# Performance work log

Hardware: AMD Instinct MI355X
Metric: run time of the kernel (lower is better)

The kernel has to match this reference:

```python
import jax, jax.numpy as jnp
import numpy as np

D = 1024      # model_dim (input_dim)
H = 2048      # hidden_size_per_expert (hardcoded in module)
E = 8         # num_experts
K = 2         # topk
T = 8192      # tokens (batch after view)


def setup_inputs() -> dict:
    key = jax.random.key(0)
    ks = jax.random.split(key, 6)
    s_in = 1.0 / np.sqrt(D)
    s_h = 1.0 / np.sqrt(H)
    return {
        "x": jax.random.normal(ks[0], (T, D), dtype=jnp.float32),
        "wg": jax.random.normal(ks[1], (D, E), dtype=jnp.float32) * s_in,   # gate Linear(D,E,bias=False)
        "w1": jax.random.normal(ks[2], (E, D, H), dtype=jnp.float32) * s_in,
        "b1": jnp.zeros((E, H), dtype=jnp.float32),
        "w2": jax.random.normal(ks[3], (E, H, D), dtype=jnp.float32) * s_h,
        "b2": jnp.zeros((E, D), dtype=jnp.float32),
    }


def _moe(x, wg, w1, b1, w2, b2):
    # top-k gating (Tutel 'top' gate, k=K)
    logits = x @ wg                         # [T,E]
    scores = jax.nn.softmax(logits, -1)     # [T,E]
    topv, topi = jax.lax.top_k(scores, K)   # [T,K]
    sel = jax.nn.one_hot(topi, E, dtype=x.dtype)          # [T,K,E]
    combine = jnp.einsum('tk,tke->te', topv, sel)          # sparse combine weights [T,E]
    # GShard-style load-balance aux loss (top-1 dispatch mask)
    ce = sel[:, 0, :].mean(0)               # fraction of tokens whose top1 is e
    me = scores.mean(0)                     # mean gate prob per expert
    l_aux = jnp.sum(me * ce) * E
    # expert FFN (dense over experts; combine zeros out non-selected)
    h = jax.nn.relu(jnp.einsum('td,edh->teh', x, w1) + b1)  # [T,E,H]
    y = jnp.einsum('teh,ehd->ted', h, w2) + b2              # [T,E,D]
    out = jnp.einsum('te,ted->td', combine, y)              # [T,D]
    return out, l_aux


def reference(x, wg, w1, b1, w2, b2):
    return _moe(x, wg, w1, b1, w2, b2)
```

## Files before the change

kernel.cpp:

```cpp
#include <hip/hip_runtime.h>
#include <stdint.h>

#define T_TOK 8192
#define DIM   1024
#define HID   2048
#define NE    8

#define BM 128
#define BN 128
#define BK 64

#define GB_TOK 32

typedef float floatx4 __attribute__((ext_vector_type(4)));
typedef short shortx8 __attribute__((ext_vector_type(8)));

typedef __attribute__((address_space(3))) void       lds_void;
typedef const __attribute__((address_space(1))) void gbl_void;

__device__ __forceinline__ unsigned short f2bf(float f) {
  unsigned int u = __float_as_uint(f);
  unsigned int r = 0x7fffu + ((u >> 16) & 1u);
  return (unsigned short)((u + r) >> 16);
}

__global__ __launch_bounds__(256) void transpose_cast_kernel(const float* __restrict__ in,
                                                             unsigned short* __restrict__ out,
                                                             int R, int C) {
  __shared__ float tile[32][33];
  const size_t eoff = (size_t)blockIdx.z * R * C;
  const float* ip = in + eoff;
  unsigned short* op = out + eoff;
  int c0 = blockIdx.x * 32, r0 = blockIdx.y * 32;
  int tx = threadIdx.x, ty = threadIdx.y;
#pragma unroll
  for (int i = 0; i < 4; i++)
    tile[ty + i * 8][tx] = ip[(size_t)(r0 + ty + i * 8) * C + (c0 + tx)];
  __syncthreads();
#pragma unroll
  for (int i = 0; i < 4; i++)
    op[(size_t)(c0 + ty + i * 8) * R + (r0 + tx)] = f2bf(tile[tx][ty + i * 8]);
}

__global__ __launch_bounds__(256) void gate_kernel(const float* __restrict__ x,
                                                   const float* __restrict__ wg,
                                                   unsigned short* __restrict__ xb,
                                                   int* counts, int* top1cnt, float* ssum,
                                                   int* tok_list, float* wgt_list) {
  __shared__ int   lds_cnt[8];
  __shared__ int   lds_top1[8];
  __shared__ float lds_ssum[4][8];
  __shared__ int   tk_e[GB_TOK][2];
  __shared__ int   tk_r[GB_TOK][2];
  __shared__ float tk_w[GB_TOK][2];
  __shared__ int   base[8];

  const int tid = threadIdx.x;
  const int wave = tid >> 6;
  const int lane = tid & 63;

  if (tid < 8) { lds_cnt[tid] = 0; lds_top1[tid] = 0; }
  if (tid < 32) lds_ssum[tid >> 3][tid & 7] = 0.f;
  __syncthreads();

  float ssum_local[8];
#pragma unroll
  for (int e = 0; e < 8; e++) ssum_local[e] = 0.f;

  for (int it = 0; it < GB_TOK / 4; it++) {
    const int lt = it * 4 + wave;
    const int t = blockIdx.x * GB_TOK + lt;

    float acc[8];
#pragma unroll
    for (int e = 0; e < 8; e++) acc[e] = 0.f;
    const float* xr = x + (size_t)t * DIM;
    unsigned short* xw = xb + (size_t)t * DIM;
#pragma unroll
    for (int i = 0; i < 16; i++) {
      int d = i * 64 + lane;
      float xv = xr[d];
      xw[d] = f2bf(xv);
      const float4* wr = reinterpret_cast<const float4*>(wg + d * 8);
      float4 w0 = wr[0], w1 = wr[1];
      acc[0] += xv * w0.x; acc[1] += xv * w0.y; acc[2] += xv * w0.z; acc[3] += xv * w0.w;
      acc[4] += xv * w1.x; acc[5] += xv * w1.y; acc[6] += xv * w1.z; acc[7] += xv * w1.w;
    }
#pragma unroll
    for (int e = 0; e < 8; e++) {
#pragma unroll
      for (int off = 32; off > 0; off >>= 1) acc[e] += __shfl_xor(acc[e], off, 64);
    }
    if (lane == 0) {
      float mx = acc[0];
#pragma unroll
      for (int e = 1; e < 8; e++) mx = fmaxf(mx, acc[e]);
      float s[8], sum = 0.f;
#pragma unroll
      for (int e = 0; e < 8; e++) { s[e] = expf(acc[e] - mx); sum += s[e]; }
      float inv = 1.f / sum;
#pragma unroll
      for (int e = 0; e < 8; e++) { s[e] *= inv; ssum_local[e] += s[e]; }
      int i1 = 0;
#pragma unroll
      for (int e = 1; e < 8; e++) if (s[e] > s[i1]) i1 = e;
      int i2 = (i1 == 0) ? 1 : 0;
#pragma unroll
      for (int e = 0; e < 8; e++) if (e != i1 && s[e] > s[i2]) i2 = e;
      atomicAdd(&lds_top1[i1], 1);
      int r1 = atomicAdd(&lds_cnt[i1], 1);
      int r2 = atomicAdd(&lds_cnt[i2], 1);
      tk_e[lt][0] = i1; tk_r[lt][0] = r1; tk_w[lt][0] = s[i1];
      tk_e[lt][1] = i2; tk_r[lt][1] = r2; tk_w[lt][1] = s[i2];
    }
  }
  if (lane == 0) {
#pragma unroll
    for (int e = 0; e < 8; e++) lds_ssum[wave][e] = ssum_local[e];
  }
  __syncthreads();
  if (tid < 8) {
    base[tid] = atomicAdd(&counts[tid], lds_cnt[tid]);
    atomicAdd(&top1cnt[tid], lds_top1[tid]);
    atomicAdd(&ssum[tid],
              lds_ssum[0][tid] + lds_ssum[1][tid] + lds_ssum[2][tid] + lds_ssum[3][tid]);
  }
  __syncthreads();
  if (tid < GB_TOK * 2) {
    int lt = tid >> 1, k = tid & 1;
    int e = tk_e[lt][k];
    int pos = base[e] + tk_r[lt][k];
    tok_list[e * T_TOK + pos] = blockIdx.x * GB_TOK + lt;
    wgt_list[e * T_TOK + pos] = tk_w[lt][k];
  }
}

__global__ void scan_kernel(const int* counts, const int* top1cnt, const float* ssum,
                            int* h_off, int* tile_off, float* laux_out) {
  if (threadIdx.x == 0 && blockIdx.x == 0) {
    int off = 0, toff = 0;
    float l = 0.f;
    for (int e = 0; e < 8; e++) {
      h_off[e] = off;
      tile_off[e] = toff;
      off += counts[e];
      toff += (counts[e] + BM - 1) / BM;
      l += (ssum[e] / (float)T_TOK) * ((float)top1cnt[e] / (float)T_TOK);
    }
    tile_off[8] = toff;
    *laux_out = l * (float)NE;
  }
}

template <int MODE>
__global__ __launch_bounds__(256, 4) void moe_gemm_kernel(
    const unsigned short* __restrict__ A_src, const unsigned short* __restrict__ B_src,
    const float* __restrict__ bias, const int* __restrict__ counts,
    const int* __restrict__ h_off, const int* __restrict__ tile_off,
    const int* __restrict__ tok_list, const float* __restrict__ wgt_list,
    unsigned short* __restrict__ h_out, float* __restrict__ out, int N, int K) {
  __shared__ unsigned short s_a[BM][BK];
  __shared__ unsigned short s_b[BN][BK];

  const int ntx = N / BN;
  const int cpx = ntx * 17;
  const int bid = blockIdx.x;
  const int wg  = (bid & 7) * cpx + (bid >> 3);
  const int bt  = wg / ntx;
  const int nt  = wg - bt * ntx;

  if (bt >= tile_off[8]) return;
  int e = 7;
#pragma unroll
  for (int q = 6; q >= 0; q--)
    if (bt < tile_off[q + 1]) e = q;
  const int n_e = counts[e];
  const int m0 = (bt - tile_off[e]) * BM;
  const int n0 = nt * BN;
  const int tid = threadIdx.x;

  const int lane = tid & 63;
  const int wv = tid >> 6;
  const int lrow = lane >> 3;
  const int lchk = (lane & 7) ^ lrow;

  const unsigned short* a_g[4];
  const unsigned short* b_g[4];
  lds_void* a_l[4];
  lds_void* b_l[4];
#pragma unroll
  for (int c = 0; c < 4; c++) {
    int ra = wv * 32 + c * 8 + lrow;
    int gr = m0 + ra;
    int safe = (gr < n_e) ? gr : (n_e - 1);
    const unsigned short* abase;
    if (MODE == 0) {
      int tok = tok_list[e * T_TOK + safe];
      abase = A_src + (size_t)tok * K;
    } else {
      abase = A_src + (size_t)(h_off[e] + safe) * K;
    }
    a_g[c] = abase + lchk * 8;
    b_g[c] = B_src + ((size_t)e * N + n0 + ra) * K + lchk * 8;
    a_l[c] = (lds_void*)&s_a[wv * 32 + c * 8][0];
    b_l[c] = (lds_void*)&s_b[wv * 32 + c * 8][0];
  }

  const int lm = lane & 15;
  const int quad = lane >> 4;
  const int r7 = lm & 7;
  const int wm = (wv >> 1) * 64;
  const int wn = (wv & 1) * 64;

  floatx4 acc[4][4];
#pragma unroll
  for (int mi = 0; mi < 4; mi++)
#pragma unroll
    for (int ni = 0; ni < 4; ni++) acc[mi][ni] = (floatx4){0.f, 0.f, 0.f, 0.f};

  for (int kt = 0; kt < K; kt += BK) {
#pragma unroll
    for (int c = 0; c < 4; c++) {
      __builtin_amdgcn_global_load_lds((gbl_void*)(a_g[c] + kt), a_l[c], 16, 0, 0);
      __builtin_amdgcn_global_load_lds((gbl_void*)(b_g[c] + kt), b_l[c], 16, 0, 0);
    }
    __syncthreads();
#pragma unroll
    for (int kk = 0; kk < 2; kk++) {
      const int pc = ((kk << 2) + quad) ^ r7;
      shortx8 af[4], bfr[4];
#pragma unroll
      for (int mi = 0; mi < 4; mi++)
        af[mi] = *reinterpret_cast<const shortx8*>(&s_a[wm + mi * 16 + lm][pc << 3]);
#pragma unroll
      for (int ni = 0; ni < 4; ni++)
        bfr[ni] = *reinterpret_cast<const shortx8*>(&s_b[wn + ni * 16 + lm][pc << 3]);
#pragma unroll
      for (int mi = 0; mi < 4; mi++)
#pragma unroll
        for (int ni = 0; ni < 4; ni++)
          acc[mi][ni] = __builtin_amdgcn_mfma_f32_16x16x32_bf16(af[mi], bfr[ni], acc[mi][ni], 0, 0, 0);
    }
    __syncthreads();
  }

#pragma unroll
  for (int mi = 0; mi < 4; mi++) {
#pragma unroll
    for (int r = 0; r < 4; r++) {
      int row = m0 + wm + mi * 16 + quad * 4 + r;
      if (row >= n_e) continue;
      if (MODE == 0) {
        size_t base = (size_t)(h_off[e] + row) * N;
#pragma unroll
        for (int ni = 0; ni < 4; ni++) {
          int col = n0 + wn + ni * 16 + lm;
          float v = acc[mi][ni][r] + bias[e * N + col];
          v = fmaxf(v, 0.f);
          h_out[base + col] = f2bf(v);
        }
      } else {
        int tok = tok_list[e * T_TOK + row];
        float wgt = wgt_list[e * T_TOK + row];
        size_t base = (size_t)tok * N;
#pragma unroll
        for (int ni = 0; ni < 4; ni++) {
          int col = n0 + wn + ni * 16 + lm;
          float v = wgt * (acc[mi][ni][r] + bias[e * N + col]);
          atomicAdd(&out[base + col], v);
        }
      }
    }
  }
}

extern "C" void kernel_launch(void* const* d_in, const int* in_sizes, int n_in,
                              void* d_out, int out_size, void* d_ws, size_t ws_size,
                              hipStream_t stream) {
  const float* x  = (const float*)d_in[0];
  const float* wg = (const float*)d_in[1];
  const float* w1 = (const float*)d_in[2];
  const float* b1 = (const float*)d_in[3];
  const float* w2 = (const float*)d_in[4];
  const float* b2 = (const float*)d_in[5];
  float* out = (float*)d_out;

  char* ws = (char*)d_ws;
  int*            counts   = (int*)(ws + 0);
  int*            top1cnt  = (int*)(ws + 32);
  float*          ssum     = (float*)(ws + 64);
  int*            h_off    = (int*)(ws + 96);
  int*            tile_off = (int*)(ws + 128);
  int*            tok_list = (int*)(ws + 256);
  float*          wgt_list = (float*)(ws + 262400);
  unsigned short* x_bf     = (unsigned short*)(ws + 524544);
  unsigned short* w1t      = (unsigned short*)(ws + 17301760);
  unsigned short* w2t      = (unsigned short*)(ws + 50856192);
  unsigned short* h_buf    = (unsigned short*)(ws + 84410624);

  hipMemsetAsync(ws, 0, 256, stream);
  hipMemsetAsync(d_out, 0, (size_t)out_size * sizeof(float), stream);

  dim3 tb(32, 8);
  transpose_cast_kernel<<<dim3(HID / 32, DIM / 32, NE), tb, 0, stream>>>(w1, w1t, DIM, HID);
  transpose_cast_kernel<<<dim3(DIM / 32, HID / 32, NE), tb, 0, stream>>>(w2, w2t, HID, DIM);

  gate_kernel<<<T_TOK / GB_TOK, 256, 0, stream>>>(x, wg, x_bf, counts, top1cnt, ssum,
                                                  tok_list, wgt_list);
  scan_kernel<<<1, 64, 0, stream>>>(counts, top1cnt, ssum, h_off, tile_off,
                                    out + (size_t)T_TOK * DIM);

  moe_gemm_kernel<0><<<dim3((HID / BN) * 136), 256, 0, stream>>>(
      x_bf, w1t, b1, counts, h_off, tile_off, tok_list, wgt_list, h_buf, nullptr, HID, DIM);
  moe_gemm_kernel<1><<<dim3((DIM / BN) * 136), 256, 0, stream>>>(
      h_buf, w2t, b2, counts, h_off, tile_off, tok_list, wgt_list, nullptr, out, DIM, HID);
}
```

Baseline: 461.1 us.

## Load MFMA fragments directly from global memory, removing LDS staging

Replaces the LDS-staged GEMM mainloop with per-wave direct global loads of A/B fragments into registers, double-buffered in software across 32-wide K steps. This removes the LDS writes and reads and the barriers per K tile, and lowers the occupancy hint to 2 blocks per SM. The cost is more global and L2 traffic, because waves no longer share the tile through LDS, and row-strided loads that coalesce less well.

```diff
diff --git a/kernel.cpp b/kernel.cpp
--- a/kernel.cpp
+++ b/kernel.cpp
@@ -8,15 +8,11 @@
 
 #define BM 128
 #define BN 128
-#define BK 64
 
 #define GB_TOK 32
 
 typedef float floatx4 __attribute__((ext_vector_type(4)));
 typedef short shortx8 __attribute__((ext_vector_type(8)));
-
-typedef __attribute__((address_space(3))) void       lds_void;
-typedef const __attribute__((address_space(1))) void gbl_void;
 
 __device__ __forceinline__ unsigned short f2bf(float f) {
   unsigned int u = __float_as_uint(f);
@@ -153,15 +149,12 @@
 }
 
 template <int MODE>
-__global__ __launch_bounds__(256, 4) void moe_gemm_kernel(
+__global__ __launch_bounds__(256, 2) void moe_gemm_kernel(
     const unsigned short* __restrict__ A_src, const unsigned short* __restrict__ B_src,
     const float* __restrict__ bias, const int* __restrict__ counts,
     const int* __restrict__ h_off, const int* __restrict__ tile_off,
     const int* __restrict__ tok_list, const float* __restrict__ wgt_list,
     unsigned short* __restrict__ h_out, float* __restrict__ out, int N, int K) {
-  __shared__ unsigned short s_a[BM][BK];
-  __shared__ unsigned short s_b[BN][BK];
-
   const int ntx = N / BN;
   const int cpx = ntx * 17;
   const int bid = blockIdx.x;
@@ -181,36 +174,26 @@
 
   const int lane = tid & 63;
   const int wv = tid >> 6;
-  const int lrow = lane >> 3;
-  const int lchk = (lane & 7) ^ lrow;
-
-  const unsigned short* a_g[4];
-  const unsigned short* b_g[4];
-  lds_void* a_l[4];
-  lds_void* b_l[4];
-#pragma unroll
-  for (int c = 0; c < 4; c++) {
-    int ra = wv * 32 + c * 8 + lrow;
-    int gr = m0 + ra;
+  const int lm = lane & 15;
+  const int quad = lane >> 4;
+  const int wm = (wv >> 1) * 64;
+  const int wn = (wv & 1) * 64;
+
+  const unsigned short* ap[4];
+  const unsigned short* bp[4];
+#pragma unroll
+  for (int x = 0; x < 4; x++) {
+    int gr = m0 + wm + x * 16 + lm;
     int safe = (gr < n_e) ? gr : (n_e - 1);
     const unsigned short* abase;
     if (MODE == 0) {
-      int tok = tok_list[e * T_TOK + safe];
-      abase = A_src + (size_t)tok * K;
+      abase = A_src + (size_t)tok_list[e * T_TOK + safe] * K;
     } else {
       abase = A_src + (size_t)(h_off[e] + safe) * K;
     }
-    a_g[c] = abase + lchk * 8;
-    b_g[c] = B_src + ((size_t)e * N + n0 + ra) * K + lchk * 8;
-    a_l[c] = (lds_void*)&s_a[wv * 32 + c * 8][0];
-    b_l[c] = (lds_void*)&s_b[wv * 32 + c * 8][0];
-  }
-
-  const int lm = lane & 15;
-  const int quad = lane >> 4;
-  const int r7 = lm & 7;
-  const int wm = (wv >> 1) * 64;
-  const int wn = (wv & 1) * 64;
+    ap[x] = abase + quad * 8;
+    bp[x] = B_src + ((size_t)e * N + n0 + wn + x * 16 + lm) * K + quad * 8;
+  }
 
   floatx4 acc[4][4];
 #pragma unroll
@@ -218,30 +201,33 @@
 #pragma unroll
     for (int ni = 0; ni < 4; ni++) acc[mi][ni] = (floatx4){0.f, 0.f, 0.f, 0.f};
 
-  for (int kt = 0; kt < K; kt += BK) {
-#pragma unroll
-    for (int c = 0; c < 4; c++) {
-      __builtin_amdgcn_global_load_lds((gbl_void*)(a_g[c] + kt), a_l[c], 16, 0, 0);
-      __builtin_amdgcn_global_load_lds((gbl_void*)(b_g[c] + kt), b_l[c], 16, 0, 0);
-    }
-    __syncthreads();
-#pragma unroll
-    for (int kk = 0; kk < 2; kk++) {
-      const int pc = ((kk << 2) + quad) ^ r7;
-      shortx8 af[4], bfr[4];
-#pragma unroll
-      for (int mi = 0; mi < 4; mi++)
-        af[mi] = *reinterpret_cast<const shortx8*>(&s_a[wm + mi * 16 + lm][pc << 3]);
-#pragma unroll
-      for (int ni = 0; ni < 4; ni++)
-        bfr[ni] = *reinterpret_cast<const shortx8*>(&s_b[wn + ni * 16 + lm][pc << 3]);
-#pragma unroll
-      for (int mi = 0; mi < 4; mi++)
-#pragma unroll
-        for (int ni = 0; ni < 4; ni++)
-          acc[mi][ni] = __builtin_amdgcn_mfma_f32_16x16x32_bf16(af[mi], bfr[ni], acc[mi][ni], 0, 0, 0);
-    }
-    __syncthreads();
+#define LOADF(Adst, Bdst, KO)                                                \
+  do {                                                                       \
+    _Pragma("unroll") for (int x_ = 0; x_ < 4; x_++) {                       \
+      Adst[x_] = *reinterpret_cast<const shortx8*>(ap[x_] + (KO));           \
+      Bdst[x_] = *reinterpret_cast<const shortx8*>(bp[x_] + (KO));           \
+    }                                                                        \
+  } while (0)
+
+#define MFMAF(Aset, Bset)                                                    \
+  do {                                                                       \
+    _Pragma("unroll") for (int mi_ = 0; mi_ < 4; mi_++)                      \
+      _Pragma("unroll") for (int ni_ = 0; ni_ < 4; ni_++)                    \
+        acc[mi_][ni_] = __builtin_amdgcn_mfma_f32_16x16x32_bf16(             \
+            Aset[mi_], Bset[ni_], acc[mi_][ni_], 0, 0, 0);                   \
+  } while (0)
+
+  const int NS = K / 32;
+  shortx8 aR[4], bR[4], aN[4], bN[4];
+
+  LOADF(aR, bR, 0);
+  for (int sb = 0; sb < NS / 2; ++sb) {
+    const int ko = sb * 64;
+    LOADF(aN, bN, ko + 32);
+    MFMAF(aR, bR);
+    const int ko2 = (ko + 64 < K) ? (ko + 64) : (K - 32);
+    LOADF(aR, bR, ko2);
+    MFMAF(aN, bN);
   }
 
 #pragma unroll
@@ -272,6 +258,8 @@
       }
     }
   }
+#undef LOADF
+#undef MFMAF
 }
 
 extern "C" void kernel_launch(void* const* d_in, const int* in_sizes, int n_in,
```

Result: slower. 850.1 us (+84.4%).
